# Optimization experiments

Measured on AMD Instinct MI355X. Metric: run time of the kernel, lower is better.

## Reference

```python
import jax, jax.numpy as jnp
import numpy as np

C, D, B = 32768, 1024, 16384
LABEL = 0.95  # EMA keep factor from __init__ default


def setup_inputs() -> dict:
    key = jax.random.key(0)
    k1, k2, k3, k4 = jax.random.split(key, 4)
    return {
        "s_logits": jax.random.normal(k1, (C, D), dtype=jnp.float32),
        "t_logits": jax.random.normal(k2, (C, D), dtype=jnp.float32),
        "logits": jax.random.normal(k3, (B, D), dtype=jnp.float32),
        "the_class": jax.random.randint(k4, (B,), 0, C, dtype=jnp.int64),
    }


def _ema_scatter(table, logits, the_class, keep):
    """Sequential per-row EMA: for i in range(B): table[c_i] = table[c_i]*keep + logits[i]*(1-keep).
    Vectorized: row c with k occurrences -> table[c]*keep^k + (1-keep)*sum_j keep^{#later occurrences} * logits[j].
    """
    Bn = the_class.shape[0]
    Cn = table.shape[0]
    dt = table.dtype
    ones = jnp.ones((Bn,), dtype=dt)
    counts = jax.ops.segment_sum(ones, the_class, num_segments=Cn)  # [C]
    # occurrence rank (0-based, in original batch order) of each sample within its class
    order = jnp.argsort(the_class)  # stable sort preserves batch order within a class
    sc = the_class[order]
    first = jnp.searchsorted(sc, sc, side="left")  # start of each class segment
    rank_sorted = jnp.arange(Bn, dtype=jnp.int32) - first.astype(jnp.int32)
    rank = jnp.zeros((Bn,), jnp.int32).at[order].set(rank_sorted)
    # number of later same-class occurrences
    r = counts[the_class] - 1.0 - rank.astype(dt)  # [B]
    w = (1.0 - keep) * jnp.power(jnp.asarray(keep, dt), r)  # [B]
    contrib = jax.ops.segment_sum(logits * w[:, None], the_class, num_segments=Cn)  # [C, D]
    decay = jnp.power(jnp.asarray(keep, dt), counts)  # [C]; rows absent from batch keep decay=1
    return table * decay[:, None] + contrib


def reference(s_logits, t_logits, logits, the_class):
    new_s = _ema_scatter(s_logits, logits, the_class, LABEL)  # update(type='s')
    loss = jnp.mean(jnp.sum(jnp.abs(new_s - t_logits), axis=1))  # loss()
    return loss
```

## Files before the change

### kernel.cpp

```cpp
#include <hip/hip_runtime.h>

#define NC 32768
#define ND 1024
#define NQ 256
#define NB 16384
#define KEEP 0.95f
#define OMK  0.05f
#define KCAP 16
#define RPB 4

typedef float f4 __attribute__((ext_vector_type(4)));

__device__ __forceinline__ void fma4(f4& a, float w, f4 b) {
    a.x = fmaf(w, b.x, a.x);
    a.y = fmaf(w, b.y, a.y);
    a.z = fmaf(w, b.z, a.z);
    a.w = fmaf(w, b.w, a.w);
}

__global__ void count_scatter_kernel(const int* __restrict__ the_class,
                                     int* __restrict__ counts,
                                     int* __restrict__ idx_list) {
    int i = blockIdx.x * blockDim.x + threadIdx.x;
    if (i < NB) {
        int c = the_class[i];
        int pos = atomicAdd(&counts[c], 1);
        if (pos < KCAP) idx_list[c * KCAP + pos] = i;
    }
}

__global__ void wprep_kernel(const int* __restrict__ counts,
                             const int* __restrict__ idx_list,
                             float* __restrict__ decays,
                             int2* __restrict__ elist) {
    int c = blockIdx.x * blockDim.x + threadIdx.x;
    int cnt = counts[c];
    float base = KEEP, r = 1.0f;
    for (int e = cnt; e > 0; e >>= 1) { if (e & 1) r *= base; base *= base; }
    decays[c] = r;
    int m = cnt < KCAP ? cnt : KCAP;
    int idx[KCAP];
    #pragma unroll
    for (int j = 0; j < KCAP; ++j)
        idx[j] = (j < m) ? idx_list[c * KCAP + j] : -1;
    #pragma unroll
    for (int j = 0; j < KCAP; ++j) {
        if (j < m) {
            int later = 0;
            #pragma unroll
            for (int l = 0; l < KCAP; ++l) later += (idx[l] > idx[j]);
            float w = OMK;
            for (int k = 0; k < later; ++k) w *= KEEP;
            int2 e; e.x = idx[j]; e.y = __float_as_int(w);
            elist[c * KCAP + j] = e;
        }
    }
}

__global__ __launch_bounds__(256, 5) void loss_kernel(
    const float* __restrict__ s_logits,
    const float* __restrict__ t_logits,
    const float* __restrict__ logits,
    const int*   __restrict__ counts,
    const float* __restrict__ decays,
    const int2*  __restrict__ elist,
    float* __restrict__ out) {

    const int q  = threadIdx.x;
    const int c0 = blockIdx.x * RPB;

    const f4* s4 = (const f4*)s_logits;
    const f4* t4 = (const f4*)t_logits;
    const f4* l4 = (const f4*)logits;

    f4 sv[RPB], tv[RPB];
    #pragma unroll
    for (int r = 0; r < RPB; ++r) sv[r] = s4[(size_t)(c0 + r) * NQ + q];
    #pragma unroll
    for (int r = 0; r < RPB; ++r) tv[r] = t4[(size_t)(c0 + r) * NQ + q];

    float dec[RPB]; int m[RPB]; int2 e0[RPB];
    #pragma unroll
    for (int r = 0; r < RPB; ++r) {
        dec[r] = decays[c0 + r];
        int cnt = counts[c0 + r];
        m[r] = cnt < KCAP ? cnt : KCAP;
        e0[r] = elist[(c0 + r) * KCAP];
    }

    f4 lv0[RPB];
    #pragma unroll
    for (int r = 0; r < RPB; ++r) {
        if (m[r] > 0) lv0[r] = l4[(size_t)e0[r].x * NQ + q];
    }

    float lsum = 0.0f;
    #pragma unroll
    for (int r = 0; r < RPB; ++r) {
        const int c = c0 + r;
        f4 acc;
        acc.x = sv[r].x * dec[r];
        acc.y = sv[r].y * dec[r];
        acc.z = sv[r].z * dec[r];
        acc.w = sv[r].w * dec[r];
        if (m[r] > 0) {
            fma4(acc, __int_as_float(e0[r].y), lv0[r]);
            for (int j = 1; j < m[r]; ++j) {
                int2 e = elist[c * KCAP + j];
                f4 lv = l4[(size_t)e.x * NQ + q];
                fma4(acc, __int_as_float(e.y), lv);
            }
        }
        lsum += fabsf(acc.x - tv[r].x) + fabsf(acc.y - tv[r].y) +
                fabsf(acc.z - tv[r].z) + fabsf(acc.w - tv[r].w);
    }

    #pragma unroll
    for (int off = 32; off > 0; off >>= 1) lsum += __shfl_down(lsum, off);
    __shared__ float wsum[4];
    const int wave = threadIdx.x >> 6, lane = threadIdx.x & 63;
    if (lane == 0) wsum[wave] = lsum;
    __syncthreads();
    if (threadIdx.x == 0) {
        float total = (wsum[0] + wsum[1] + wsum[2] + wsum[3]) * (1.0f / NC);
        atomicAdd(out, total);
    }
}

extern "C" void kernel_launch(void* const* d_in, const int* in_sizes, int n_in,
                              void* d_out, int out_size, void* d_ws, size_t ws_size,
                              hipStream_t stream) {
    const float* s_logits  = (const float*)d_in[0];
    const float* t_logits  = (const float*)d_in[1];
    const float* logits    = (const float*)d_in[2];
    const int*   the_class = (const int*)d_in[3];
    float* out = (float*)d_out;

    int*   counts   = (int*)d_ws;
    int*   idx_list = counts + NC;
    float* decays   = (float*)(idx_list + NC * KCAP);
    int2*  elist    = (int2*)(decays + NC);

    hipMemsetAsync(counts, 0, NC * sizeof(int), stream);
    hipMemsetAsync(d_out, 0, sizeof(float), stream);

    count_scatter_kernel<<<NB / 256, 256, 0, stream>>>(the_class, counts, idx_list);
    wprep_kernel<<<NC / 256, 256, 0, stream>>>(counts, idx_list, decays, elist);
    loss_kernel<<<NC / RPB, 256, 0, stream>>>(s_logits, t_logits, logits,
                                              counts, decays, elist, out);
}
```

Measured before the change: 345.4 us.

## Make loss kernel persistent with double-buffered prefetch of next row group

The loss kernel now launches a fixed 1024 blocks, and each block loops over 8 groups of 4 class rows instead of one group per block. While the current group is computed, the next group's s_logits rows and metadata are prefetched into alternate register buffers. This is meant to hide memory latency and cut block launch and tail overhead for a bandwidth-bound reduction. In exchange it raises register pressure, removes the occupancy hint from the launch bounds, and with fewer blocks there may be less parallelism to saturate HBM.

New measurement: 350.0 us. No clear change (+1.3%).

```diff
diff --git a/kernel.cpp b/kernel.cpp
--- a/kernel.cpp
+++ b/kernel.cpp
@@ -8,6 +8,8 @@
 #define OMK  0.05f
 #define KCAP 16
 #define RPB 4
+#define BLOCKS 1024
+#define TPB (NC / RPB / BLOCKS)
 
 typedef float f4 __attribute__((ext_vector_type(4)));
 
@@ -57,7 +59,7 @@
     }
 }
 
-__global__ __launch_bounds__(256, 5) void loss_kernel(
+__global__ __launch_bounds__(256) void loss_kernel(
     const float* __restrict__ s_logits,
     const float* __restrict__ t_logits,
     const float* __restrict__ logits,
@@ -66,54 +68,88 @@
     const int2*  __restrict__ elist,
     float* __restrict__ out) {
 
-    const int q  = threadIdx.x;
-    const int c0 = blockIdx.x * RPB;
-
+    const int q = threadIdx.x;
     const f4* s4 = (const f4*)s_logits;
     const f4* t4 = (const f4*)t_logits;
     const f4* l4 = (const f4*)logits;
 
-    f4 sv[RPB], tv[RPB];
-    #pragma unroll
-    for (int r = 0; r < RPB; ++r) sv[r] = s4[(size_t)(c0 + r) * NQ + q];
-    #pragma unroll
-    for (int r = 0; r < RPB; ++r) tv[r] = t4[(size_t)(c0 + r) * NQ + q];
+    f4 svA[RPB], svB[RPB], tv[RPB], lv[RPB];
+    float decA[RPB], decB[RPB];
+    int   mA[RPB],  mB[RPB];
+    int2  eA[RPB],  eB[RPB];
 
-    float dec[RPB]; int m[RPB]; int2 e0[RPB];
-    #pragma unroll
-    for (int r = 0; r < RPB; ++r) {
-        dec[r] = decays[c0 + r];
-        int cnt = counts[c0 + r];
-        m[r] = cnt < KCAP ? cnt : KCAP;
-        e0[r] = elist[(c0 + r) * KCAP];
+    const int base0 = blockIdx.x * (TPB * RPB);
+    float lsum = 0.0f;
+
+#define LOAD_META(DEC, M, E, base)                                  \
+    _Pragma("unroll")                                               \
+    for (int r = 0; r < RPB; ++r) {                                 \
+        DEC[r] = decays[(base) + r];                                \
+        int cnt = counts[(base) + r];                               \
+        M[r] = cnt < KCAP ? cnt : KCAP;                             \
+        E[r] = elist[((base) + r) * KCAP];                          \
     }
 
-    f4 lv0[RPB];
-    #pragma unroll
-    for (int r = 0; r < RPB; ++r) {
-        if (m[r] > 0) lv0[r] = l4[(size_t)e0[r].x * NQ + q];
+#define LOAD_SV(SV, base)                                           \
+    _Pragma("unroll")                                               \
+    for (int r = 0; r < RPB; ++r)                                   \
+        SV[r] = s4[(size_t)((base) + r) * NQ + q];
+
+#define ISSUE_CUR(M, E, base)                                       \
+    _Pragma("unroll")                                               \
+    for (int r = 0; r < RPB; ++r)                                   \
+        if (M[r] > 0) lv[r] = l4[(size_t)E[r].x * NQ + q];          \
+    _Pragma("unroll")                                               \
+    for (int r = 0; r < RPB; ++r)                                   \
+        tv[r] = t4[(size_t)((base) + r) * NQ + q];
+
+#define COMPUTE(SV, DEC, M, E, base)                                \
+    _Pragma("unroll")                                               \
+    for (int r = 0; r < RPB; ++r) {                                 \
+        f4 acc;                                                     \
+        acc.x = SV[r].x * DEC[r];                                   \
+        acc.y = SV[r].y * DEC[r];                                   \
+        acc.z = SV[r].z * DEC[r];                                   \
+        acc.w = SV[r].w * DEC[r];                                   \
+        if (M[r] > 0) {                                             \
+            fma4(acc, __int_as_float(E[r].y), lv[r]);               \
+            for (int j = 1; j < M[r]; ++j) {      \
+                int2 e = elist[((base) + r) * KCAP + j];            \
+                f4 g = l4[(size_t)e.x * NQ + q];                    \
+                fma4(acc, __int_as_float(e.y), g);                  \
+            }                                                       \
+        }                                                           \
+        lsum += fabsf(acc.x - tv[r].x) + fabsf(acc.y - tv[r].y) +   \
+                fabsf(acc.z - tv[r].z) + fabsf(acc.w - tv[r].w);    \
     }
 
-    float lsum = 0.0f;
+    LOAD_META(decA, mA, eA, base0);
+    LOAD_SV(svA, base0);
+
     #pragma unroll
-    for (int r = 0; r < RPB; ++r) {
-        const int c = c0 + r;
-        f4 acc;
-        acc.x = sv[r].x * dec[r];
-        acc.y = sv[r].y * dec[r];
-        acc.z = sv[r].z * dec[r];
-        acc.w = sv[r].w * dec[r];
-        if (m[r] > 0) {
-            fma4(acc, __int_as_float(e0[r].y), lv0[r]);
-            for (int j = 1; j < m[r]; ++j) {
-                int2 e = elist[c * KCAP + j];
-                f4 lv = l4[(size_t)e.x * NQ + q];
-                fma4(acc, __int_as_float(e.y), lv);
+    for (int i = 0; i < TPB; ++i) {
+        const int cc = base0 + i * RPB;
+        if ((i & 1) == 0) {
+            ISSUE_CUR(mA, eA, cc);
+            if (i < TPB - 1) {
+                LOAD_META(decB, mB, eB, cc + RPB);
+                LOAD_SV(svB, cc + RPB);
             }
+            COMPUTE(svA, decA, mA, eA, cc);
+        } else {
+            ISSUE_CUR(mB, eB, cc);
+            if (i < TPB - 1) {
+                LOAD_META(decA, mA, eA, cc + RPB);
+                LOAD_SV(svA, cc + RPB);
+            }
+            COMPUTE(svB, decB, mB, eB, cc);
         }
-        lsum += fabsf(acc.x - tv[r].x) + fabsf(acc.y - tv[r].y) +
-                fabsf(acc.z - tv[r].z) + fabsf(acc.w - tv[r].w);
     }
+
+#undef LOAD_META
+#undef LOAD_SV
+#undef ISSUE_CUR
+#undef COMPUTE
 
     #pragma unroll
     for (int off = 32; off > 0; off >>= 1) lsum += __shfl_down(lsum, off);
@@ -146,6 +182,6 @@
 
     count_scatter_kernel<<<NB / 256, 256, 0, stream>>>(the_class, counts, idx_list);
     wprep_kernel<<<NC / 256, 256, 0, stream>>>(counts, idx_list, decays, elist);
-    loss_kernel<<<NC / RPB, 256, 0, stream>>>(s_logits, t_logits, logits,
-                                              counts, decays, elist, out);
+    loss_kernel<<<BLOCKS, 256, 0, stream>>>(s_logits, t_logits, logits,
+                                            counts, decays, elist, out);
 }
```

## Split rows into branchless common path and separate rare-row kernel with prefetch

Applied to the files above, without the earlier changes.

The loss kernel becomes a persistent grid-stride loop over rows. Each iteration reads a packed per-row metadata record (decay, up to two weights and indices, gate), prefetches the next row's s/t/meta, and always loads two logits rows, so the inner loop has no data-dependent branching. Rows with more than two occurrences get gate zero there and are handled by a separate rare_kernel, fed by an atomically built list. In exchange it adds a kernel launch and an extra atomic pass. It also always issues two logits loads per row, falling back to row 0 for empty slots, which adds wasted reads for rows absent from the batch.

Result: no change. 351.9 us (+1.9%).

```diff
diff --git a/kernel.cpp b/kernel.cpp
--- a/kernel.cpp
+++ b/kernel.cpp
@@ -7,16 +7,12 @@
 #define KEEP 0.95f
 #define OMK  0.05f
 #define KCAP 16
-#define RPB 4
+#define GRID 2048
+#define RPT (NC / GRID)
+#define RARE_GRID 4096
 
 typedef float f4 __attribute__((ext_vector_type(4)));
-
-__device__ __forceinline__ void fma4(f4& a, float w, f4 b) {
-    a.x = fmaf(w, b.x, a.x);
-    a.y = fmaf(w, b.y, a.y);
-    a.z = fmaf(w, b.z, a.z);
-    a.w = fmaf(w, b.w, a.w);
-}
+typedef float f8 __attribute__((ext_vector_type(8)));
 
 __global__ void count_scatter_kernel(const int* __restrict__ the_class,
                                      int* __restrict__ counts,
@@ -31,18 +27,20 @@
 
 __global__ void wprep_kernel(const int* __restrict__ counts,
                              const int* __restrict__ idx_list,
-                             float* __restrict__ decays,
-                             int2* __restrict__ elist) {
+                             f8* __restrict__ row_meta,
+                             int2* __restrict__ elist,
+                             int* __restrict__ rare_list,
+                             int* __restrict__ rare_cnt) {
     int c = blockIdx.x * blockDim.x + threadIdx.x;
     int cnt = counts[c];
     float base = KEEP, r = 1.0f;
     for (int e = cnt; e > 0; e >>= 1) { if (e & 1) r *= base; base *= base; }
-    decays[c] = r;
     int m = cnt < KCAP ? cnt : KCAP;
     int idx[KCAP];
     #pragma unroll
     for (int j = 0; j < KCAP; ++j)
         idx[j] = (j < m) ? idx_list[c * KCAP + j] : -1;
+    float w0 = 0.0f, w1 = 0.0f; int i0 = 0, i1 = 0;
     #pragma unroll
     for (int j = 0; j < KCAP; ++j) {
         if (j < m) {
@@ -53,66 +51,71 @@
             for (int k = 0; k < later; ++k) w *= KEEP;
             int2 e; e.x = idx[j]; e.y = __float_as_int(w);
             elist[c * KCAP + j] = e;
+            if (j == 0) { w0 = w; i0 = idx[j]; }
+            if (j == 1) { w1 = w; i1 = idx[j]; }
         }
     }
-}
-
-__global__ __launch_bounds__(256, 5) void loss_kernel(
+    f8 me;
+    me[0] = r;
+    if (cnt > 2) {
+        int p = atomicAdd(rare_cnt, 1);
+        rare_list[p] = c;
+        me[1] = 0.0f; me[2] = __int_as_float(0);
+        me[3] = 0.0f; me[4] = __int_as_float(0);
+        me[5] = 0.0f;
+    } else {
+        me[1] = w0; me[2] = __int_as_float(i0);
+        me[3] = w1; me[4] = __int_as_float(i1);
+        me[5] = 1.0f;
+    }
+    me[6] = 0.0f; me[7] = 0.0f;
+    row_meta[c] = me;
+}
+
+__global__ __launch_bounds__(256) void loss_kernel(
     const float* __restrict__ s_logits,
     const float* __restrict__ t_logits,
     const float* __restrict__ logits,
-    const int*   __restrict__ counts,
-    const float* __restrict__ decays,
-    const int2*  __restrict__ elist,
+    const f8*    __restrict__ row_meta,
     float* __restrict__ out) {
 
-    const int q  = threadIdx.x;
-    const int c0 = blockIdx.x * RPB;
-
+    const int q = threadIdx.x;
     const f4* s4 = (const f4*)s_logits;
     const f4* t4 = (const f4*)t_logits;
     const f4* l4 = (const f4*)logits;
 
-    f4 sv[RPB], tv[RPB];
-    #pragma unroll
-    for (int r = 0; r < RPB; ++r) sv[r] = s4[(size_t)(c0 + r) * NQ + q];
-    #pragma unroll
-    for (int r = 0; r < RPB; ++r) tv[r] = t4[(size_t)(c0 + r) * NQ + q];
-
-    float dec[RPB]; int m[RPB]; int2 e0[RPB];
-    #pragma unroll
-    for (int r = 0; r < RPB; ++r) {
-        dec[r] = decays[c0 + r];
-        int cnt = counts[c0 + r];
-        m[r] = cnt < KCAP ? cnt : KCAP;
-        e0[r] = elist[(c0 + r) * KCAP];
-    }
-
-    f4 lv0[RPB];
-    #pragma unroll
-    for (int r = 0; r < RPB; ++r) {
-        if (m[r] > 0) lv0[r] = l4[(size_t)e0[r].x * NQ + q];
-    }
+    int row = blockIdx.x;
+
+    f8 me = row_meta[row];
+    f4 sv = s4[(size_t)row * NQ + q];
+    f4 tv = t4[(size_t)row * NQ + q];
+    f4 lv0 = l4[(size_t)__float_as_int(me[2]) * NQ + q];
+    f4 lv1 = l4[(size_t)__float_as_int(me[4]) * NQ + q];
 
     float lsum = 0.0f;
-    #pragma unroll
-    for (int r = 0; r < RPB; ++r) {
-        const int c = c0 + r;
+    #pragma unroll 1
+    for (int k = 0; k < RPT; ++k) {
+        const int rown = row + GRID;
+        f8 meN; f4 svN, tvN;
+        if (k < RPT - 1) {
+            meN = row_meta[rown];
+            svN = s4[(size_t)rown * NQ + q];
+            tvN = t4[(size_t)rown * NQ + q];
+        }
+        const float dec = me[0], w0 = me[1], w1 = me[3], gate = me[5];
         f4 acc;
-        acc.x = sv[r].x * dec[r];
-        acc.y = sv[r].y * dec[r];
-        acc.z = sv[r].z * dec[r];
-        acc.w = sv[r].w * dec[r];
-        if (m[r] > 0) {
-            fma4(acc, __int_as_float(e0[r].y), lv0[r]);
-            for (int j = 1; j < m[r]; ++j) {
-                int2 e = elist[c * KCAP + j];
-                f4 lv = l4[(size_t)e.x * NQ + q];
-                fma4(acc, __int_as_float(e.y), lv);
-            }
+        acc.x = fmaf(w1, lv1.x, fmaf(w0, lv0.x, sv.x * dec));
+        acc.y = fmaf(w1, lv1.y, fmaf(w0, lv0.y, sv.y * dec));
+        acc.z = fmaf(w1, lv1.z, fmaf(w0, lv0.z, sv.z * dec));
+        acc.w = fmaf(w1, lv1.w, fmaf(w0, lv0.w, sv.w * dec));
+        const float rs = fabsf(acc.x - tv.x) + fabsf(acc.y - tv.y) +
+                         fabsf(acc.z - tv.z) + fabsf(acc.w - tv.w);
+        lsum = fmaf(gate, rs, lsum);
+        if (k < RPT - 1) {
+            lv0 = l4[(size_t)__float_as_int(meN[2]) * NQ + q];
+            lv1 = l4[(size_t)__float_as_int(meN[4]) * NQ + q];
+            me = meN; sv = svN; tv = tvN; row = rown;
         }
-        lsum += fabsf(acc.x - tv[r].x) + fabsf(acc.y - tv[r].y) +
-                fabsf(acc.z - tv[r].z) + fabsf(acc.w - tv[r].w);
     }
 
     #pragma unroll
@@ -127,6 +130,59 @@
     }
 }
 
+__global__ __launch_bounds__(256) void rare_kernel(
+    const float* __restrict__ s_logits,
+    const float* __restrict__ t_logits,
+    const float* __restrict__ logits,
+    const int*   __restrict__ counts,
+    const f8*    __restrict__ row_meta,
+    const int2*  __restrict__ elist,
+    const int*   __restrict__ rare_list,
+    const int*   __restrict__ rare_cnt,
+    float* __restrict__ out) {
+
+    const int b = blockIdx.x;
+    if (b >= *rare_cnt) return;
+    const int c = rare_list[b];
+    const int q = threadIdx.x;
+
+    const f4* s4 = (const f4*)s_logits;
+    const f4* t4 = (const f4*)t_logits;
+    const f4* l4 = (const f4*)logits;
+
+    const int cnt = counts[c];
+    const int m = cnt < KCAP ? cnt : KCAP;
+    const float dec = row_meta[c][0];
+
+    f4 sv = s4[(size_t)c * NQ + q];
+    f4 tv = t4[(size_t)c * NQ + q];
+    f4 acc;
+    acc.x = sv.x * dec; acc.y = sv.y * dec;
+    acc.z = sv.z * dec; acc.w = sv.w * dec;
+    for (int j = 0; j < m; ++j) {
+        int2 e = elist[c * KCAP + j];
+        const float w = __int_as_float(e.y);
+        f4 lv = l4[(size_t)e.x * NQ + q];
+        acc.x = fmaf(w, lv.x, acc.x);
+        acc.y = fmaf(w, lv.y, acc.y);
+        acc.z = fmaf(w, lv.z, acc.z);
+        acc.w = fmaf(w, lv.w, acc.w);
+    }
+    float lsum = fabsf(acc.x - tv.x) + fabsf(acc.y - tv.y) +
+                 fabsf(acc.z - tv.z) + fabsf(acc.w - tv.w);
+
+    #pragma unroll
+    for (int off = 32; off > 0; off >>= 1) lsum += __shfl_down(lsum, off);
+    __shared__ float wsum[4];
+    const int wave = threadIdx.x >> 6, lane = threadIdx.x & 63;
+    if (lane == 0) wsum[wave] = lsum;
+    __syncthreads();
+    if (threadIdx.x == 0) {
+        float total = (wsum[0] + wsum[1] + wsum[2] + wsum[3]) * (1.0f / NC);
+        atomicAdd(out, total);
+    }
+}
+
 extern "C" void kernel_launch(void* const* d_in, const int* in_sizes, int n_in,
                               void* d_out, int out_size, void* d_ws, size_t ws_size,
                               hipStream_t stream) {
@@ -136,16 +192,20 @@
     const int*   the_class = (const int*)d_in[3];
     float* out = (float*)d_out;
 
-    int*   counts   = (int*)d_ws;
-    int*   idx_list = counts + NC;
-    float* decays   = (float*)(idx_list + NC * KCAP);
-    int2*  elist    = (int2*)(decays + NC);
-
-    hipMemsetAsync(counts, 0, NC * sizeof(int), stream);
+    int*  counts    = (int*)d_ws;
+    int*  rare_cnt  = counts + NC;
+    int*  idx_list  = counts + NC + 4;
+    f8*   row_meta  = (f8*)(idx_list + NC * KCAP);
+    int2* elist     = (int2*)(row_meta + NC);
+    int*  rare_list = (int*)(elist + NC * KCAP);
+
+    hipMemsetAsync(counts, 0, (NC + 4) * sizeof(int), stream);
     hipMemsetAsync(d_out, 0, sizeof(float), stream);
 
     count_scatter_kernel<<<NB / 256, 256, 0, stream>>>(the_class, counts, idx_list);
-    wprep_kernel<<<NC / 256, 256, 0, stream>>>(counts, idx_list, decays, elist);
-    loss_kernel<<<NC / RPB, 256, 0, stream>>>(s_logits, t_logits, logits,
-                                              counts, decays, elist, out);
-}
+    wprep_kernel<<<NC / 256, 256, 0, stream>>>(counts, idx_list, row_meta, elist,
+                                               rare_list, rare_cnt);
+    loss_kernel<<<GRID, 256, 0, stream>>>(s_logits, t_logits, logits, row_meta, out);
+    rare_kernel<<<RARE_GRID, 256, 0, stream>>>(s_logits, t_logits, logits, counts,
+                                               row_meta, elist, rare_list, rare_cnt, out);
+}
```
